# Optimization experiments

Measured on AMD Instinct MI355X. Metric: run time of the kernel, lower is better.

The kernel has to match this reference:

```python
import jax, jax.numpy as jnp
import numpy as np

EMB = 1024
HEAD = 64

def setup_inputs() -> dict:
    key = jax.random.key(0)
    k1, k2, k3, k4, k5 = jax.random.split(key, 5)
    x = jax.random.normal(k1, (4, 4096, EMB), dtype=jnp.float32)
    # qkv linear: weight [3*HEAD, EMB] torch-style -> store as [EMB, 3*HEAD]
    W_qkv = jax.random.normal(k2, (EMB, 3 * HEAD), dtype=jnp.float32) * (1.0 / np.sqrt(EMB))
    b_qkv = jax.random.normal(k3, (3 * HEAD,), dtype=jnp.float32) * 0.01
    W_out = jax.random.normal(k4, (HEAD, EMB), dtype=jnp.float32) * (1.0 / np.sqrt(HEAD))
    b_out = jax.random.normal(k5, (EMB,), dtype=jnp.float32) * 0.01
    return {"x": x, "W_qkv": W_qkv, "b_qkv": b_qkv, "W_out": W_out, "b_out": b_out}

def reference(x, W_qkv, b_qkv, W_out, b_out):
    qkv = jnp.einsum('bse,ed->bsd', x, W_qkv) + b_qkv            # [B,S,3H]
    q, k, v = jnp.split(qkv, 3, axis=-1)                          # each [B,S,H]
    scale = 1.0 / jnp.sqrt(jnp.asarray(q.shape[-1], q.dtype))
    scores = jnp.einsum('bqh,bkh->bqk', q, k) * scale             # [B,S,S]
    attn = jax.nn.softmax(scores, axis=-1)
    ctx = jnp.einsum('bqk,bkh->bqh', attn, v)                     # [B,S,H]
    return jnp.einsum('bqh,he->bqe', ctx, W_out) + b_out          # [B,S,E]
```

## Files before the change

### kernel.cpp

```cpp
#include <hip/hip_runtime.h>
#include <hip/hip_bf16.h>


#define LD 72

typedef __attribute__((ext_vector_type(8))) short short8;
typedef __attribute__((ext_vector_type(4))) short short4v;
typedef __attribute__((ext_vector_type(4))) float floatx4;

#define MFMA(a, b, c) __builtin_amdgcn_mfma_f32_16x16x32_bf16((a), (b), (c), 0, 0, 0)

__device__ __forceinline__ unsigned short f2bf(float f) {
  union { float f; unsigned u; } c; c.f = f;
  unsigned u = c.u + 0x7fffu + ((c.u >> 16) & 1u);
  return (unsigned short)(u >> 16);
}
__device__ __forceinline__ float asf(unsigned u) {
  union { unsigned u; float f; } c; c.u = u; return c.f;
}

__global__ __launch_bounds__(256) void prep_kernel(
    const float* __restrict__ Wqkv, const float* __restrict__ Wout,
    unsigned short* __restrict__ WtQkv, unsigned short* __restrict__ WtOut) {
  int idx = blockIdx.x * 256 + threadIdx.x;
  if (idx < 192 * 1024) {
    int n = idx >> 10, k = idx & 1023;
    WtQkv[idx] = f2bf(Wqkv[k * 192 + n]);
  } else if (idx < 192 * 1024 + 1024 * 64) {
    int j = idx - 192 * 1024;
    int e = j >> 6, d = j & 63;
    WtOut[j] = f2bf(Wout[d * 1024 + e]);
  }
}

__global__ __launch_bounds__(256, 2) void qkv_kernel(
    const float* __restrict__ x, const unsigned short* __restrict__ WtQkv,
    const float* __restrict__ bqkv,
    unsigned short* __restrict__ Qg, unsigned short* __restrict__ Kg,
    unsigned short* __restrict__ Vtg) {
  __shared__ __align__(16) unsigned short XS[2][32 * LD];
  __shared__ __align__(16) unsigned short WS[2][192 * LD];

  const int tid = threadIdx.x;
  const int wave = tid >> 6, lane = tid & 63, quad = lane >> 4, l16 = lane & 15;
  const int row0 = blockIdx.x * 32;
  const int colbase = wave * 48;

  floatx4 acc[2][3];
#pragma unroll
  for (int rt = 0; rt < 2; rt++)
#pragma unroll
    for (int t = 0; t < 3; t++) acc[rt][t] = (floatx4)(0.0f);

  const int xr = tid >> 3, xj = tid & 7;
  const float* gx = x + (size_t)(row0 + xr) * 1024 + xj * 8;
  const unsigned short* gw = WtQkv + (size_t)xr * 1024 + xj * 8;

  {
    float4 xa = *(const float4*)(gx);
    float4 xb = *(const float4*)(gx + 4);
    uint4 wv[6];
#pragma unroll
    for (int i = 0; i < 6; i++) wv[i] = *(const uint4*)(gw + i * 32768);
    short8 xc;
    xc[0] = (short)f2bf(xa.x); xc[1] = (short)f2bf(xa.y);
    xc[2] = (short)f2bf(xa.z); xc[3] = (short)f2bf(xa.w);
    xc[4] = (short)f2bf(xb.x); xc[5] = (short)f2bf(xb.y);
    xc[6] = (short)f2bf(xb.z); xc[7] = (short)f2bf(xb.w);
    *(short8*)(&XS[0][xr * LD + xj * 8]) = xc;
#pragma unroll
    for (int i = 0; i < 6; i++)
      *(uint4*)(&WS[0][(xr + 32 * i) * LD + xj * 8]) = wv[i];
  }
  __syncthreads();

  for (int kc = 0; kc < 16; kc++) {
    const int buf = kc & 1;
    float4 nxa, nxb;
    uint4 nwv[6];
    if (kc < 15) {
      const float* gxn = gx + (kc + 1) * 64;
      nxa = *(const float4*)(gxn);
      nxb = *(const float4*)(gxn + 4);
      const unsigned short* gwn = gw + (kc + 1) * 64;
#pragma unroll
      for (int i = 0; i < 6; i++) nwv[i] = *(const uint4*)(gwn + i * 32768);
    }
    short8 a0 = *(const short8*)(&XS[buf][l16 * LD + quad * 8]);
    short8 a0h = *(const short8*)(&XS[buf][l16 * LD + 32 + quad * 8]);
    short8 a1 = *(const short8*)(&XS[buf][(16 + l16) * LD + quad * 8]);
    short8 a1h = *(const short8*)(&XS[buf][(16 + l16) * LD + 32 + quad * 8]);
#pragma unroll
    for (int t = 0; t < 3; t++) {
      short8 b0 = *(const short8*)(&WS[buf][(colbase + t * 16 + l16) * LD + quad * 8]);
      short8 b1 = *(const short8*)(&WS[buf][(colbase + t * 16 + l16) * LD + 32 + quad * 8]);
      acc[0][t] = MFMA(a0, b0, acc[0][t]);
      acc[0][t] = MFMA(a0h, b1, acc[0][t]);
      acc[1][t] = MFMA(a1, b0, acc[1][t]);
      acc[1][t] = MFMA(a1h, b1, acc[1][t]);
    }
    if (kc < 15) {
      short8 xc;
      xc[0] = (short)f2bf(nxa.x); xc[1] = (short)f2bf(nxa.y);
      xc[2] = (short)f2bf(nxa.z); xc[3] = (short)f2bf(nxa.w);
      xc[4] = (short)f2bf(nxb.x); xc[5] = (short)f2bf(nxb.y);
      xc[6] = (short)f2bf(nxb.z); xc[7] = (short)f2bf(nxb.w);
      *(short8*)(&XS[buf ^ 1][xr * LD + xj * 8]) = xc;
#pragma unroll
      for (int i = 0; i < 6; i++)
        *(uint4*)(&WS[buf ^ 1][(xr + 32 * i) * LD + xj * 8]) = nwv[i];
    }
    __syncthreads();
  }

  unsigned short* eQ = &XS[0][0];
  unsigned short* eK = &XS[1][0];
  unsigned short* eV = &WS[0][0];
  const int b = row0 >> 12, srow = row0 & 4095;
#pragma unroll
  for (int rt = 0; rt < 2; rt++)
#pragma unroll
    for (int t = 0; t < 3; t++) {
      int col = colbase + t * 16 + l16;
      float bias = bqkv[col];
      int sec = col >> 6, d = col & 63;
#pragma unroll
      for (int r = 0; r < 4; r++) {
        int lrow = rt * 16 + quad * 4 + r;
        float v = acc[rt][t][r] + bias;
        if (sec == 0)      eQ[lrow * LD + d] = f2bf(v * 0.125f);
        else if (sec == 1) eK[lrow * LD + d] = f2bf(v);
        else               eV[d * 40 + lrow] = f2bf(v);
      }
    }
  __syncthreads();
  {
    int r = tid >> 3, sg = tid & 7;
    *(uint4*)(Qg + (size_t)(row0 + r) * 64 + sg * 8) = *(const uint4*)(&eQ[r * LD + sg * 8]);
    *(uint4*)(Kg + (size_t)(row0 + r) * 64 + sg * 8) = *(const uint4*)(&eK[r * LD + sg * 8]);
  }
  {
    const int g = srow >> 6, k0 = (srow & 63) >> 4;
    int d = tid >> 2, i4 = tid & 3;
    unsigned short* vb = Vtg + (((size_t)b * 64 + g) * 64 + d) * 64 + k0;
#pragma unroll
    for (int ii = 0; ii < 4; ii++) {
      int idx = i4 * 4 + ii;
      unsigned lo = eV[d * 40 + idx];
      unsigned hi = eV[d * 40 + 16 + idx];
      *(unsigned*)(vb + idx * 4) = lo | (hi << 16);
    }
  }
}

__global__ __launch_bounds__(256, 4) void attn_kernel(
    const unsigned short* __restrict__ Qg, const unsigned short* __restrict__ Kg,
    const unsigned short* __restrict__ Vtg,
    unsigned short* __restrict__ Opart, float* __restrict__ Lpart) {
  __shared__ __align__(16) unsigned short Ks[64 * LD];
  __shared__ __align__(16) unsigned short Vs[64 * LD];
  __shared__ __align__(16) unsigned short QP[64 * LD];

  const int tid = threadIdx.x;
  const int wave = tid >> 6, lane = tid & 63, quad = lane >> 4, l16 = lane & 15;
  const int bid = blockIdx.x;
  const int combo = bid & 15, qt = bid >> 4;
  const int b = combo >> 2, split = combo & 3;
  const int q0 = qt * 64, key0 = split * 1024;

  {
    int r = tid >> 2, seg = tid & 3;
    const uint4* s = (const uint4*)(Qg + ((size_t)b * 4096 + q0 + r) * 64 + seg * 16);
    *(uint4*)(&QP[r * LD + seg * 16])     = s[0];
    *(uint4*)(&QP[r * LD + seg * 16 + 8]) = s[1];
  }
  short8 aq0 = *(const short8*)(&QP[(wave * 16 + l16) * LD + quad * 8]);
  short8 aq1 = *(const short8*)(&QP[(wave * 16 + l16) * LD + 32 + quad * 8]);

  floatx4 o[4];
  float lsum[4];
#pragma unroll
  for (int t = 0; t < 4; t++) o[t] = (floatx4)(0.0f);
#pragma unroll
  for (int r = 0; r < 4; r++) lsum[r] = 0.0f;

  const int kr = tid >> 2, kseg = tid & 3;
  const unsigned short* Kbase = Kg + ((size_t)b * 4096 + key0) * 64;
  const unsigned short* Vt0 = Vtg + ((size_t)b * 64 + (key0 >> 6)) * 4096;

  uint4 pk0, pk1, pv0, pv1;
  pk0 = *(const uint4*)(Kbase + (size_t)kr * 64 + kseg * 16);
  pk1 = *(const uint4*)(Kbase + (size_t)kr * 64 + kseg * 16 + 8);
  pv0 = *(const uint4*)(Vt0 + (size_t)kr * 64 + kseg * 16);
  pv1 = *(const uint4*)(Vt0 + (size_t)kr * 64 + kseg * 16 + 8);

  unsigned short* Pw = &QP[wave * 16 * LD];

  for (int kc = 0; kc < 16; kc++) {
    __syncthreads();
    *(uint4*)(&Ks[kr * LD + kseg * 16])     = pk0;
    *(uint4*)(&Ks[kr * LD + kseg * 16 + 8]) = pk1;
    *(uint4*)(&Vs[kr * LD + kseg * 16])     = pv0;
    *(uint4*)(&Vs[kr * LD + kseg * 16 + 8]) = pv1;
    __syncthreads();
    if (kc < 15) {
      int nk = (kc + 1) * 64;
      pk0 = *(const uint4*)(Kbase + (size_t)(nk + kr) * 64 + kseg * 16);
      pk1 = *(const uint4*)(Kbase + (size_t)(nk + kr) * 64 + kseg * 16 + 8);
      pv0 = *(const uint4*)(Vt0 + (size_t)(kc + 1) * 4096 + kr * 64 + kseg * 16);
      pv1 = *(const uint4*)(Vt0 + (size_t)(kc + 1) * 4096 + kr * 64 + kseg * 16 + 8);
    }

    floatx4 sc[4];
#pragma unroll
    for (int t = 0; t < 4; t++) sc[t] = (floatx4)(0.0f);
#pragma unroll
    for (int t = 0; t < 4; t++) {
      short8 b0 = *(const short8*)(&Ks[(t * 16 + l16) * LD + quad * 8]);
      short8 b1 = *(const short8*)(&Ks[(t * 16 + l16) * LD + 32 + quad * 8]);
      sc[t] = MFMA(aq0, b0, sc[t]);
      sc[t] = MFMA(aq1, b1, sc[t]);
    }

#pragma unroll
    for (int r = 0; r < 4; r++) {
      float e0 = __expf(sc[0][r]);
      float e1 = __expf(sc[1][r]);
      float e2 = __expf(sc[2][r]);
      float e3 = __expf(sc[3][r]);
      lsum[r] += (e0 + e1) + (e2 + e3);
      unsigned w0, w1;
      asm("v_cvt_pk_bf16_f32 %0, %1, %2" : "=v"(w0) : "v"(e0), "v"(e1));
      asm("v_cvt_pk_bf16_f32 %0, %1, %2" : "=v"(w1) : "v"(e2), "v"(e3));
      uint2 pw; pw.x = w0; pw.y = w1;
      *(uint2*)(&Pw[(quad * 4 + r) * LD + l16 * 4]) = pw;
    }
    short8 ap0 = *(const short8*)(&Pw[l16 * LD + quad * 8]);
    short8 ap1 = *(const short8*)(&Pw[l16 * LD + 32 + quad * 8]);
#pragma unroll
    for (int t = 0; t < 4; t++) {
      short8 b0 = *(const short8*)(&Vs[(t * 16 + l16) * LD + quad * 8]);
      short8 b1 = *(const short8*)(&Vs[(t * 16 + l16) * LD + 32 + quad * 8]);
      o[t] = MFMA(ap0, b0, o[t]);
      o[t] = MFMA(ap1, b1, o[t]);
    }
  }

#pragma unroll
  for (int r = 0; r < 4; r++) {
#pragma unroll
    for (int off = 1; off < 16; off <<= 1) lsum[r] += __shfl_xor(lsum[r], off, 64);
  }

  unsigned short* Ob = Opart + ((size_t)bid * 64 + wave * 16) * 64;
#pragma unroll
  for (int t = 0; t < 4; t++)
#pragma unroll
    for (int r = 0; r < 4; r++)
      Ob[(quad * 4 + r) * 64 + t * 16 + l16] = f2bf(o[t][r]);
  if (l16 == 0) {
#pragma unroll
    for (int r = 0; r < 4; r++)
      Lpart[bid * 64 + wave * 16 + quad * 4 + r] = lsum[r];
  }
}

__global__ __launch_bounds__(256, 4) void combine_kernel(
    const unsigned short* __restrict__ Opart, const float* __restrict__ Lpart,
    const unsigned short* __restrict__ WtOut, const float* __restrict__ bout,
    float* __restrict__ out) {
  __shared__ __align__(16) unsigned short Cs[4][16 * LD];
  __shared__ __align__(16) unsigned short Wl[128 * LD];

  const int tid = threadIdx.x;
  const int wave = tid >> 6, lane = tid & 63, quad = lane >> 4, l16 = lane & 15;
  const int cid = blockIdx.x;
  const int eq = cid & 3, qt = (cid >> 2) & 63, b = cid >> 8;
  const int e0 = eq * 256;

  const int q = lane >> 2, d0 = (lane & 3) * 16;
  float accv[16];
#pragma unroll
  for (int i = 0; i < 16; i++) accv[i] = 0.0f;
  float lq = 0.0f;
#pragma unroll
  for (int s = 0; s < 4; s++) {
    int pid = qt * 16 + b * 4 + s;
    const unsigned short* src = Opart + ((size_t)pid * 64 + wave * 16 + q) * 64 + d0;
    uint4 h0 = *(const uint4*)src;
    uint4 h1 = *(const uint4*)(src + 8);
    const unsigned* hw = (const unsigned*)&h0;
#pragma unroll
    for (int i = 0; i < 4; i++) {
      accv[2 * i]     += asf(hw[i] << 16);
      accv[2 * i + 1] += asf(hw[i] & 0xFFFF0000u);
    }
    const unsigned* hw1 = (const unsigned*)&h1;
#pragma unroll
    for (int i = 0; i < 4; i++) {
      accv[8 + 2 * i]     += asf(hw1[i] << 16);
      accv[8 + 2 * i + 1] += asf(hw1[i] & 0xFFFF0000u);
    }
    lq += Lpart[pid * 64 + wave * 16 + q];
  }
  float inv = 1.0f / lq;
  short8 c0, c1;
#pragma unroll
  for (int i = 0; i < 8; i++) {
    c0[i] = (short)f2bf(accv[i] * inv);
    c1[i] = (short)f2bf(accv[8 + i] * inv);
  }
  *(short8*)(&Cs[wave][q * LD + d0])     = c0;
  *(short8*)(&Cs[wave][q * LD + d0 + 8]) = c1;
  short8 ao0 = *(const short8*)(&Cs[wave][l16 * LD + quad * 8]);
  short8 ao1 = *(const short8*)(&Cs[wave][l16 * LD + 32 + quad * 8]);

  const size_t orow0 = (size_t)b * 4096 + qt * 64 + wave * 16;
#pragma unroll 1
  for (int ec = 0; ec < 2; ec++) {
    int ebase = e0 + ec * 128;
    __syncthreads();
    {
      int er = tid >> 1, half = tid & 1;
      const uint4* s = (const uint4*)(WtOut + (size_t)(ebase + er) * 64 + half * 32);
      uint4 w0 = s[0], w1 = s[1], w2 = s[2], w3 = s[3];
      *(uint4*)(&Wl[er * LD + half * 32])      = w0;
      *(uint4*)(&Wl[er * LD + half * 32 + 8])  = w1;
      *(uint4*)(&Wl[er * LD + half * 32 + 16]) = w2;
      *(uint4*)(&Wl[er * LD + half * 32 + 24]) = w3;
    }
    __syncthreads();
    floatx4 a2[8];
#pragma unroll
    for (int t = 0; t < 8; t++) a2[t] = (floatx4)(0.0f);
#pragma unroll
    for (int t = 0; t < 8; t++) {
      short8 b0 = *(const short8*)(&Wl[(t * 16 + l16) * LD + quad * 8]);
      short8 b1 = *(const short8*)(&Wl[(t * 16 + l16) * LD + 32 + quad * 8]);
      a2[t] = MFMA(ao0, b0, a2[t]);
      a2[t] = MFMA(ao1, b1, a2[t]);
    }
#pragma unroll
    for (int t = 0; t < 8; t++) {
      int e = ebase + t * 16 + l16;
      float bo = bout[e];
#pragma unroll
      for (int r = 0; r < 4; r++)
        out[(orow0 + quad * 4 + r) * 1024 + e] = a2[t][r] + bo;
    }
  }
}

extern "C" void kernel_launch(void* const* d_in, const int* in_sizes, int n_in,
                              void* d_out, int out_size, void* d_ws, size_t ws_size,
                              hipStream_t stream) {
  const float* x    = (const float*)d_in[0];
  const float* Wqkv = (const float*)d_in[1];
  const float* bqkv = (const float*)d_in[2];
  const float* Wout = (const float*)d_in[3];
  const float* bout = (const float*)d_in[4];
  float* out = (float*)d_out;

  unsigned short* ws = (unsigned short*)d_ws;
  unsigned short* Qg    = ws;
  unsigned short* Kg    = Qg + 1048576;
  unsigned short* Vtg   = Kg + 1048576;
  unsigned short* WtQkv = Vtg + 1048576;
  unsigned short* WtOut = WtQkv + 196608;
  unsigned short* Opart = WtOut + 65536;
  float*          Lpart = (float*)(Opart + 4194304);

  prep_kernel<<<1024, 256, 0, stream>>>(Wqkv, Wout, WtQkv, WtOut);
  qkv_kernel<<<512, 256, 0, stream>>>(x, WtQkv, bqkv, Qg, Kg, Vtg);
  attn_kernel<<<1024, 256, 0, stream>>>(Qg, Kg, Vtg, Opart, Lpart);
  combine_kernel<<<1024, 256, 0, stream>>>(Opart, Lpart, WtOut, bout, out);
}
```

Measured before the change: 180.9 us.

## Load K/V MFMA operands directly from global memory, drop LDS staging and barriers

The attention kernel no longer stages K and V tiles through shared memory. Each wave now reads its MFMA B-operands straight from global memory, which removes the LDS writes and both __syncthreads per key chunk and frees LDS for occupancy. In exchange, each of the four waves fetches the same K/V data independently (relying on L1/L2 hits), and the register double-buffered prefetch is gone, so global load latency now sits directly in front of the MFMAs.

```diff
diff --git a/kernel.cpp b/kernel.cpp
--- a/kernel.cpp
+++ b/kernel.cpp
@@ -157,8 +157,6 @@
     const unsigned short* __restrict__ Qg, const unsigned short* __restrict__ Kg,
     const unsigned short* __restrict__ Vtg,
     unsigned short* __restrict__ Opart, float* __restrict__ Lpart) {
-  __shared__ __align__(16) unsigned short Ks[64 * LD];
-  __shared__ __align__(16) unsigned short Vs[64 * LD];
   __shared__ __align__(16) unsigned short QP[64 * LD];
 
   const int tid = threadIdx.x;
@@ -184,42 +182,24 @@
 #pragma unroll
   for (int r = 0; r < 4; r++) lsum[r] = 0.0f;
 
-  const int kr = tid >> 2, kseg = tid & 3;
-  const unsigned short* Kbase = Kg + ((size_t)b * 4096 + key0) * 64;
-  const unsigned short* Vt0 = Vtg + ((size_t)b * 64 + (key0 >> 6)) * 4096;
-
-  uint4 pk0, pk1, pv0, pv1;
-  pk0 = *(const uint4*)(Kbase + (size_t)kr * 64 + kseg * 16);
-  pk1 = *(const uint4*)(Kbase + (size_t)kr * 64 + kseg * 16 + 8);
-  pv0 = *(const uint4*)(Vt0 + (size_t)kr * 64 + kseg * 16);
-  pv1 = *(const uint4*)(Vt0 + (size_t)kr * 64 + kseg * 16 + 8);
+  const unsigned short* Kb = Kg + ((size_t)b * 4096 + key0) * 64 + l16 * 64 + quad * 8;
+  const unsigned short* Vb = Vtg + ((size_t)b * 64 + (key0 >> 6)) * 4096 + l16 * 64 + quad * 8;
 
   unsigned short* Pw = &QP[wave * 16 * LD];
 
   for (int kc = 0; kc < 16; kc++) {
-    __syncthreads();
-    *(uint4*)(&Ks[kr * LD + kseg * 16])     = pk0;
-    *(uint4*)(&Ks[kr * LD + kseg * 16 + 8]) = pk1;
-    *(uint4*)(&Vs[kr * LD + kseg * 16])     = pv0;
-    *(uint4*)(&Vs[kr * LD + kseg * 16 + 8]) = pv1;
-    __syncthreads();
-    if (kc < 15) {
-      int nk = (kc + 1) * 64;
-      pk0 = *(const uint4*)(Kbase + (size_t)(nk + kr) * 64 + kseg * 16);
-      pk1 = *(const uint4*)(Kbase + (size_t)(nk + kr) * 64 + kseg * 16 + 8);
-      pv0 = *(const uint4*)(Vt0 + (size_t)(kc + 1) * 4096 + kr * 64 + kseg * 16);
-      pv1 = *(const uint4*)(Vt0 + (size_t)(kc + 1) * 4096 + kr * 64 + kseg * 16 + 8);
-    }
+    const unsigned short* kp = Kb + (size_t)kc * 4096;
+    const unsigned short* vp = Vb + (size_t)kc * 4096;
 
     floatx4 sc[4];
 #pragma unroll
     for (int t = 0; t < 4; t++) sc[t] = (floatx4)(0.0f);
 #pragma unroll
     for (int t = 0; t < 4; t++) {
-      short8 b0 = *(const short8*)(&Ks[(t * 16 + l16) * LD + quad * 8]);
-      short8 b1 = *(const short8*)(&Ks[(t * 16 + l16) * LD + 32 + quad * 8]);
-      sc[t] = MFMA(aq0, b0, sc[t]);
-      sc[t] = MFMA(aq1, b1, sc[t]);
+      short8 kb0 = *(const short8*)(kp + t * 1024);
+      short8 kb1 = *(const short8*)(kp + t * 1024 + 32);
+      sc[t] = MFMA(aq0, kb0, sc[t]);
+      sc[t] = MFMA(aq1, kb1, sc[t]);
     }
 
 #pragma unroll
@@ -239,10 +219,10 @@
     short8 ap1 = *(const short8*)(&Pw[l16 * LD + 32 + quad * 8]);
 #pragma unroll
     for (int t = 0; t < 4; t++) {
-      short8 b0 = *(const short8*)(&Vs[(t * 16 + l16) * LD + quad * 8]);
-      short8 b1 = *(const short8*)(&Vs[(t * 16 + l16) * LD + 32 + quad * 8]);
-      o[t] = MFMA(ap0, b0, o[t]);
-      o[t] = MFMA(ap1, b1, o[t]);
+      short8 vb0 = *(const short8*)(vp + t * 1024);
+      short8 vb1 = *(const short8*)(vp + t * 1024 + 32);
+      o[t] = MFMA(ap0, vb0, o[t]);
+      o[t] = MFMA(ap1, vb1, o[t]);
     }
   }
 
```

Result: slower. 264.3 us (+46.1%).
